# Kernel optimization log

Measured on AMD Instinct MI355X. Metric: run time of the kernel, lower is better.

Reference implementation:

```python
import jax, jax.numpy as jnp
import numpy as np

B, A, C, G = 32, 8732, 201, 50
NEG_TO_POS_RATIO = 3
MIN_NEG_SAMPLES = 0
DET_W, VAL_W = 0.5, 0.5
BOX_W = (10.0, 10.0, 5.0, 5.0)  # torchvision SSD BoxCoder weights


def _rand_boxes(key, shape_prefix):
    k1, k2 = jax.random.split(key)
    cxcy = jax.random.uniform(k1, shape_prefix + (2,)) * 300.0
    wh = jax.random.uniform(k2, shape_prefix + (2,)) * 90.0 + 10.0
    return jnp.concatenate([cxcy - 0.5 * wh, cxcy + 0.5 * wh], axis=-1)


def setup_inputs() -> dict:
    key = jax.random.key(0)
    ks = jax.random.split(key, 8)
    boxes = _rand_boxes(ks[0], (B, G))
    labels = jax.random.randint(ks[1], (B, G), 1, C, dtype=jnp.int32)  # foreground labels > 0
    image_label = jax.random.randint(ks[2], (B,), 0, 2, dtype=jnp.int32)
    bbox_regression = jax.random.normal(ks[3], (B, A, 4), dtype=jnp.float32)
    cls_logits = jax.random.normal(ks[4], (B, A, C), dtype=jnp.float32)
    rejection_logits = jax.random.normal(ks[5], (B, 2), dtype=jnp.float32)
    anchors = _rand_boxes(ks[6], (B, A))
    k7a, k7b = jax.random.split(ks[7])
    fg = jax.random.uniform(k7a, (B, A)) < 0.02
    gt_idx = jax.random.randint(k7b, (B, A), 0, G, dtype=jnp.int32)
    matched_idxs = jnp.where(fg, gt_idx, -1).astype(jnp.int32)
    return {"boxes": boxes, "labels": labels, "image_label": image_label,
            "bbox_regression": bbox_regression, "cls_logits": cls_logits,
            "rejection_logits": rejection_logits, "anchors": anchors,
            "matched_idxs": matched_idxs}


def _encode(gt, anc):
    # torchvision BoxCoder.encode_single with weights (10,10,5,5); boxes are xyxy
    aw = anc[..., 2] - anc[..., 0]
    ah = anc[..., 3] - anc[..., 1]
    acx = anc[..., 0] + 0.5 * aw
    acy = anc[..., 1] + 0.5 * ah
    gw = gt[..., 2] - gt[..., 0]
    gh = gt[..., 3] - gt[..., 1]
    gcx = gt[..., 0] + 0.5 * gw
    gcy = gt[..., 1] + 0.5 * gh
    wx, wy, ww, wh = BOX_W
    return jnp.stack([wx * (gcx - acx) / aw,
                      wy * (gcy - acy) / ah,
                      ww * jnp.log(gw / aw),
                      wh * jnp.log(gh / ah)], axis=-1)


def _forward(boxes, bbox_regression, cls_logits, rejection_logits, anchors,
             labels, image_label, matched_idxs):
    fg = matched_idxs >= 0                                  # [B,A]
    safe = jnp.clip(matched_idxs, 0)                        # in-range gather idx
    num_foreground = fg.sum()

    mg_boxes = jnp.take_along_axis(boxes, safe[..., None], axis=1)  # [B,A,4]
    target_reg = _encode(mg_boxes, anchors)
    d = bbox_regression - target_reg
    ad = jnp.abs(d)
    sl1 = jnp.where(ad < 1.0, 0.5 * d * d, ad - 0.5)        # beta=1.0
    bbox_loss = jnp.sum(sl1 * fg[..., None].astype(sl1.dtype), axis=(1, 2))  # [B]

    # --- classification targets + per-anchor CE ---
    cls_targets = jnp.where(fg, jnp.take_along_axis(labels, safe, axis=1), 0)  # [B,A]
    logp = jax.nn.log_softmax(cls_logits, axis=-1)
    cls_loss = -jnp.take_along_axis(logp, cls_targets[..., None], axis=-1)[..., 0]  # [B,A]

    # --- hard negative mining via double-argsort ranking ---
    fg_mask = cls_targets > 0
    num_neg = NEG_TO_POS_RATIO * fg_mask.sum(axis=1, keepdims=True)
    num_neg = jnp.where(num_neg == 0, MIN_NEG_SAMPLES, num_neg)
    neg_loss = jnp.where(fg_mask, -jnp.inf, cls_loss)
    rank = jnp.argsort(jnp.argsort(-neg_loss, axis=1), axis=1)  # descending rank
    bg_mask = rank < num_neg

    N = jnp.maximum(1, num_foreground).astype(cls_loss.dtype)
    images_without_boxes = (cls_targets.sum(axis=1) == 0).sum()
    N_neg = (MIN_NEG_SAMPLES * images_without_boxes).astype(cls_loss.dtype)

    regression_loss = bbox_loss.sum() / N
    classification_loss = (jnp.sum(jnp.where(fg_mask, cls_loss, 0.0)) +
                           jnp.sum(jnp.where(bg_mask, cls_loss, 0.0))) / (N + N_neg)

    # --- validation head loss ---
    val_logp = jax.nn.log_softmax(rejection_logits, axis=-1)
    validation_loss = -jnp.take_along_axis(val_logp, image_label[:, None], axis=-1).mean()

    loss = DET_W * (regression_loss + classification_loss) + VAL_W * validation_loss
    return jnp.stack([loss, regression_loss, classification_loss, validation_loss])


def reference(boxes, labels, image_label, bbox_regression, cls_logits,
              rejection_logits, anchors, matched_idxs):
    return _forward(boxes, bbox_regression, cls_logits, rejection_logits, anchors,
                    labels, image_label, matched_idxs)
```

## Files before the change

### kernel.cpp

```cpp
#include <hip/hip_runtime.h>
#include <math.h>

#define Bn 32
#define An 8732
#define Cn 201
#define Gn 50

#define RPB 16
#define NTILES ((An + RPB - 1) / RPB)

__device__ __forceinline__ unsigned int f2key(float f) {
    unsigned int u = __float_as_uint(f);
    return (u & 0x80000000u) ? ~u : (u | 0x80000000u);
}
__device__ __forceinline__ float key2f(unsigned int k) {
    return (k & 0x80000000u) ? __uint_as_float(k & 0x7FFFFFFFu) : __uint_as_float(~k);
}
__device__ __forceinline__ float smooth_l1(float d) {
    float ad = fabsf(d);
    return ad < 1.0f ? 0.5f * d * d : ad - 0.5f;
}

__global__ void init_kernel(int* fg_count, float* fg_cls_sum, float* bbox_sum) {
    int i = threadIdx.x;
    if (i < Bn) { fg_count[i] = 0; fg_cls_sum[i] = 0.f; bbox_sum[i] = 0.f; }
}

__global__ __launch_bounds__(256) void cls_kernel(
        const float* __restrict__ cls_logits,
        const int*   __restrict__ matched_idxs,
        const int*   __restrict__ labels,
        const float* __restrict__ boxes,
        const float* __restrict__ anchors,
        const float* __restrict__ bbox_regression,
        float* __restrict__ neg_loss,
        int*   __restrict__ fg_count,
        float* __restrict__ fg_cls_sum,
        float* __restrict__ bbox_sum) {
    __shared__ float tile[RPB * Cn];
    int b     = blockIdx.y;
    int tile0 = blockIdx.x * RPB;
    int rows  = An - tile0; if (rows > RPB) rows = RPB;
    int nvec  = rows * Cn / 4;

    const float4* g  = (const float4*)(cls_logits + ((size_t)b * An + tile0) * Cn);
    float4*       t4 = (float4*)tile;
    for (int i = threadIdx.x; i < nvec; i += 256) t4[i] = g[i];
    __syncthreads();

    int r   = threadIdx.x >> 4;
    int sub = threadIdx.x & 15;
    if (r >= rows) return;
    const float* row = tile + r * Cn;

    float v[13];
    #pragma unroll
    for (int j = 0; j < 12; ++j) v[j] = row[sub + 16 * j];
    bool has12 = (sub < Cn - 192);
    v[12] = has12 ? row[sub + 192] : -INFINITY;

    float mx = v[0];
    #pragma unroll
    for (int j = 1; j < 13; ++j) mx = fmaxf(mx, v[j]);
    #pragma unroll
    for (int off = 8; off; off >>= 1) mx = fmaxf(mx, __shfl_xor(mx, off, 64));

    float s = 0.f;
    #pragma unroll
    for (int j = 0; j < 12; ++j) s += __expf(v[j] - mx);
    if (has12) s += __expf(v[12] - mx);
    #pragma unroll
    for (int off = 8; off; off >>= 1) s += __shfl_xor(s, off, 64);

    if (sub == 0) {
        size_t row_idx = (size_t)b * An + tile0 + r;
        float lse = mx + __logf(s);
        int   mi  = matched_idxs[row_idx];
        bool  fg  = (mi >= 0);
        int   t   = fg ? labels[b * Gn + mi] : 0;
        float cl  = lse - row[t];
        if (fg) {
            neg_loss[row_idx] = -INFINITY;
            atomicAdd(&fg_cls_sum[b], cl);
            atomicAdd(&fg_count[b], 1);
            const float* gt = boxes           + (size_t)(b * Gn + mi) * 4;
            const float* an = anchors         + row_idx * 4;
            const float* rg = bbox_regression + row_idx * 4;
            float aw  = an[2] - an[0], ah  = an[3] - an[1];
            float acx = an[0] + 0.5f * aw, acy = an[1] + 0.5f * ah;
            float gw  = gt[2] - gt[0], gh  = gt[3] - gt[1];
            float gcx = gt[0] + 0.5f * gw, gcy = gt[1] + 0.5f * gh;
            float t0 = 10.f * (gcx - acx) / aw;
            float t1 = 10.f * (gcy - acy) / ah;
            float t2 = 5.f * __logf(gw / aw);
            float t3 = 5.f * __logf(gh / ah);
            float sum = smooth_l1(rg[0] - t0) + smooth_l1(rg[1] - t1)
                      + smooth_l1(rg[2] - t2) + smooth_l1(rg[3] - t3);
            atomicAdd(&bbox_sum[b], sum);
        } else {
            neg_loss[row_idx] = cl;
        }
    }
}

#define MIT 9
__global__ __launch_bounds__(1024) void mining_kernel(
        const float* __restrict__ neg_loss,
        const int*   __restrict__ fg_count,
        float* __restrict__ topk_batch) {
    int b    = blockIdx.x;
    int tid  = threadIdx.x;
    int lane = tid & 63;
    __shared__ int   cnts[32];
    __shared__ float sh_sum;
    __shared__ int   sh_cnt;

    int fc = fg_count[b];
    int k  = 3 * fc;
    int nneg = An - fc;
    if (k > nneg) k = nneg;
    if (k <= 0) {
        if (tid == 0) topk_batch[b] = 0.f;
        return;
    }

    const float* vals = neg_loss + (size_t)b * An;
    unsigned int key[MIT];
    #pragma unroll
    for (int j = 0; j < MIT; ++j) {
        int i = tid + j * 1024;
        key[j] = (i < An) ? f2key(vals[i]) : 0u;
    }

    if (tid < 32) cnts[tid] = 0;
    if (tid == 0) { sh_sum = 0.f; sh_cnt = 0; }
    __syncthreads();

    unsigned int T = 0u;
    for (int bit = 31; bit >= 0; --bit) {
        unsigned int cand = T | (1u << bit);
        int c = 0;
        #pragma unroll
        for (int j = 0; j < MIT; ++j) c += (key[j] >= cand);
        #pragma unroll
        for (int off = 32; off; off >>= 1) c += __shfl_xor(c, off, 64);
        if (lane == 0) atomicAdd(&cnts[bit], c);
        __syncthreads();
        if (cnts[bit] >= k) T = cand;
    }

    float fs = 0.f; int cgt = 0;
    #pragma unroll
    for (int j = 0; j < MIT; ++j)
        if (key[j] > T) { fs += key2f(key[j]); cgt++; }
    #pragma unroll
    for (int off = 32; off; off >>= 1) {
        fs  += __shfl_xor(fs,  off, 64);
        cgt += __shfl_xor(cgt, off, 64);
    }
    if (lane == 0) { atomicAdd(&sh_sum, fs); atomicAdd(&sh_cnt, cgt); }
    __syncthreads();
    if (tid == 0)
        topk_batch[b] = sh_sum + (float)(k - sh_cnt) * key2f(T);
}

__global__ void finalize_kernel(
        const int*   __restrict__ fg_count,
        const float* __restrict__ fg_cls_sum,
        const float* __restrict__ bbox_sum,
        const float* __restrict__ topk_batch,
        const float* __restrict__ rejection_logits,
        const int*   __restrict__ image_label,
        float* __restrict__ out) {
    int lane = threadIdx.x;
    int   fc = (lane < Bn) ? fg_count[lane]   : 0;
    float tk = (lane < Bn) ? topk_batch[lane] : 0.f;
    float cs = (lane < Bn) ? fg_cls_sum[lane] : 0.f;
    float bs = (lane < Bn) ? bbox_sum[lane]   : 0.f;
    float vl = 0.f;
    if (lane < Bn) {
        float r0 = rejection_logits[lane * 2];
        float r1 = rejection_logits[lane * 2 + 1];
        float m  = fmaxf(r0, r1);
        float lse = m + __logf(__expf(r0 - m) + __expf(r1 - m));
        vl = lse - ((image_label[lane] == 0) ? r0 : r1);
    }
    #pragma unroll
    for (int off = 32; off; off >>= 1) {
        fc += __shfl_xor(fc, off, 64);
        tk += __shfl_xor(tk, off, 64);
        cs += __shfl_xor(cs, off, 64);
        bs += __shfl_xor(bs, off, 64);
        vl += __shfl_xor(vl, off, 64);
    }
    if (lane == 0) {
        float N   = (float)((fc > 1) ? fc : 1);
        float reg = bs / N;
        float cls = (cs + tk) / N;
        float val = vl / (float)Bn;
        float loss = 0.5f * (reg + cls) + 0.5f * val;
        out[0] = loss; out[1] = reg; out[2] = cls; out[3] = val;
    }
}

extern "C" void kernel_launch(void* const* d_in, const int* in_sizes, int n_in,
                              void* d_out, int out_size, void* d_ws, size_t ws_size,
                              hipStream_t stream) {
    const float* boxes            = (const float*)d_in[0];
    const int*   labels           = (const int*)  d_in[1];
    const int*   image_label      = (const int*)  d_in[2];
    const float* bbox_regression  = (const float*)d_in[3];
    const float* cls_logits       = (const float*)d_in[4];
    const float* rejection_logits = (const float*)d_in[5];
    const float* anchors          = (const float*)d_in[6];
    const int*   matched_idxs     = (const int*)  d_in[7];
    float* out = (float*)d_out;

    float* neg_loss   = (float*)d_ws;
    int*   fg_count   = (int*)(neg_loss + Bn * An);
    float* fg_cls_sum = (float*)(fg_count + Bn);
    float* bbox_sum   = fg_cls_sum + Bn;
    float* topk_batch = bbox_sum + Bn;

    init_kernel<<<1, 64, 0, stream>>>(fg_count, fg_cls_sum, bbox_sum);

    dim3 grid(NTILES, Bn);
    cls_kernel<<<grid, 256, 0, stream>>>(cls_logits, matched_idxs, labels,
                                         boxes, anchors, bbox_regression,
                                         neg_loss, fg_count, fg_cls_sum, bbox_sum);

    mining_kernel<<<Bn, 1024, 0, stream>>>(neg_loss, fg_count, topk_batch);

    finalize_kernel<<<1, 64, 0, stream>>>(fg_count, fg_cls_sum, bbox_sum, topk_batch,
                                          rejection_logits, image_label, out);
}
```

Measured before the change: 354.1 us.

## Fuse all stages into one persistent cooperative kernel with grid syncs

```diff
diff --git a/kernel.cpp b/kernel.cpp
--- a/kernel.cpp
+++ b/kernel.cpp
@@ -1,5 +1,8 @@
 #include <hip/hip_runtime.h>
+#include <hip/hip_cooperative_groups.h>
 #include <math.h>
+
+namespace cg = cooperative_groups;
 
 #define Bn 32
 #define An 8732
@@ -8,6 +11,9 @@
 
 #define RPB 16
 #define NTILES ((An + RPB - 1) / RPB)
+#define TOTTILES (NTILES * Bn)
+#define GRID 1024
+#define MIT 35
 
 __device__ __forceinline__ unsigned int f2key(float f) {
     unsigned int u = __float_as_uint(f);
@@ -20,217 +26,266 @@
     float ad = fabsf(d);
     return ad < 1.0f ? 0.5f * d * d : ad - 0.5f;
 }
-
-__global__ void init_kernel(int* fg_count, float* fg_cls_sum, float* bbox_sum) {
-    int i = threadIdx.x;
-    if (i < Bn) { fg_count[i] = 0; fg_cls_sum[i] = 0.f; bbox_sum[i] = 0.f; }
-}
-
-__global__ __launch_bounds__(256) void cls_kernel(
+__device__ __forceinline__ void st_u32(unsigned int* p, unsigned int v) {
+    __hip_atomic_store(p, v, __ATOMIC_RELAXED, __HIP_MEMORY_SCOPE_AGENT);
+}
+__device__ __forceinline__ unsigned int ld_u32(const unsigned int* p) {
+    return __hip_atomic_load(p, __ATOMIC_RELAXED, __HIP_MEMORY_SCOPE_AGENT);
+}
+__device__ __forceinline__ void st_i32(int* p, int v) {
+    __hip_atomic_store(p, v, __ATOMIC_RELAXED, __HIP_MEMORY_SCOPE_AGENT);
+}
+__device__ __forceinline__ int ld_i32(const int* p) {
+    return __hip_atomic_load(p, __ATOMIC_RELAXED, __HIP_MEMORY_SCOPE_AGENT);
+}
+__device__ __forceinline__ void st_f32(float* p, float v) {
+    __hip_atomic_store(p, v, __ATOMIC_RELAXED, __HIP_MEMORY_SCOPE_AGENT);
+}
+__device__ __forceinline__ float ld_f32(const float* p) {
+    return __hip_atomic_load(p, __ATOMIC_RELAXED, __HIP_MEMORY_SCOPE_AGENT);
+}
+
+__global__ __launch_bounds__(256, 4) void fused_kernel(
         const float* __restrict__ cls_logits,
         const int*   __restrict__ matched_idxs,
         const int*   __restrict__ labels,
         const float* __restrict__ boxes,
         const float* __restrict__ anchors,
         const float* __restrict__ bbox_regression,
-        float* __restrict__ neg_loss,
-        int*   __restrict__ fg_count,
-        float* __restrict__ fg_cls_sum,
-        float* __restrict__ bbox_sum) {
+        const float* __restrict__ rejection_logits,
+        const int*   __restrict__ image_label,
+        unsigned int* neg_key,
+        int*   slot_cnt,
+        float* slot_cls,
+        float* slot_bbox,
+        int*   batch_fc,
+        float* batch_cls,
+        float* batch_bbox,
+        float* topk,
+        float* out) {
     __shared__ float tile[RPB * Cn];
-    int b     = blockIdx.y;
-    int tile0 = blockIdx.x * RPB;
-    int rows  = An - tile0; if (rows > RPB) rows = RPB;
-    int nvec  = rows * Cn / 4;
-
-    const float4* g  = (const float4*)(cls_logits + ((size_t)b * An + tile0) * Cn);
-    float4*       t4 = (float4*)tile;
-    for (int i = threadIdx.x; i < nvec; i += 256) t4[i] = g[i];
-    __syncthreads();
-
-    int r   = threadIdx.x >> 4;
-    int sub = threadIdx.x & 15;
-    if (r >= rows) return;
-    const float* row = tile + r * Cn;
-
-    float v[13];
-    #pragma unroll
-    for (int j = 0; j < 12; ++j) v[j] = row[sub + 16 * j];
-    bool has12 = (sub < Cn - 192);
-    v[12] = has12 ? row[sub + 192] : -INFINITY;
-
-    float mx = v[0];
-    #pragma unroll
-    for (int j = 1; j < 13; ++j) mx = fmaxf(mx, v[j]);
-    #pragma unroll
-    for (int off = 8; off; off >>= 1) mx = fmaxf(mx, __shfl_xor(mx, off, 64));
-
-    float s = 0.f;
-    #pragma unroll
-    for (int j = 0; j < 12; ++j) s += __expf(v[j] - mx);
-    if (has12) s += __expf(v[12] - mx);
-    #pragma unroll
-    for (int off = 8; off; off >>= 1) s += __shfl_xor(s, off, 64);
-
-    if (sub == 0) {
-        size_t row_idx = (size_t)b * An + tile0 + r;
-        float lse = mx + __logf(s);
-        int   mi  = matched_idxs[row_idx];
-        bool  fg  = (mi >= 0);
-        int   t   = fg ? labels[b * Gn + mi] : 0;
-        float cl  = lse - row[t];
-        if (fg) {
-            neg_loss[row_idx] = -INFINITY;
-            atomicAdd(&fg_cls_sum[b], cl);
-            atomicAdd(&fg_count[b], 1);
-            const float* gt = boxes           + (size_t)(b * Gn + mi) * 4;
-            const float* an = anchors         + row_idx * 4;
-            const float* rg = bbox_regression + row_idx * 4;
-            float aw  = an[2] - an[0], ah  = an[3] - an[1];
-            float acx = an[0] + 0.5f * aw, acy = an[1] + 0.5f * ah;
-            float gw  = gt[2] - gt[0], gh  = gt[3] - gt[1];
-            float gcx = gt[0] + 0.5f * gw, gcy = gt[1] + 0.5f * gh;
-            float t0 = 10.f * (gcx - acx) / aw;
-            float t1 = 10.f * (gcy - acy) / ah;
-            float t2 = 5.f * __logf(gw / aw);
-            float t3 = 5.f * __logf(gh / ah);
-            float sum = smooth_l1(rg[0] - t0) + smooth_l1(rg[1] - t1)
-                      + smooth_l1(rg[2] - t2) + smooth_l1(rg[3] - t3);
-            atomicAdd(&bbox_sum[b], sum);
-        } else {
-            neg_loss[row_idx] = cl;
-        }
-    }
-}
-
-#define MIT 9
-__global__ __launch_bounds__(1024) void mining_kernel(
-        const float* __restrict__ neg_loss,
-        const int*   __restrict__ fg_count,
-        float* __restrict__ topk_batch) {
-    int b    = blockIdx.x;
+    __shared__ int   p_cnt[Bn];
+    __shared__ float p_cls[Bn];
+    __shared__ float p_bbox[Bn];
+    __shared__ int   cnts[32];
+    __shared__ int   red_i;
+    __shared__ float red_f1, red_f2;
+
+    cg::grid_group gridg = cg::this_grid();
+    int bid  = blockIdx.x;
     int tid  = threadIdx.x;
     int lane = tid & 63;
-    __shared__ int   cnts[32];
-    __shared__ float sh_sum;
-    __shared__ int   sh_cnt;
-
-    int fc = fg_count[b];
-    int k  = 3 * fc;
-    int nneg = An - fc;
-    if (k > nneg) k = nneg;
-    if (k <= 0) {
-        if (tid == 0) topk_batch[b] = 0.f;
-        return;
-    }
-
-    const float* vals = neg_loss + (size_t)b * An;
-    unsigned int key[MIT];
-    #pragma unroll
-    for (int j = 0; j < MIT; ++j) {
-        int i = tid + j * 1024;
-        key[j] = (i < An) ? f2key(vals[i]) : 0u;
-    }
-
-    if (tid < 32) cnts[tid] = 0;
-    if (tid == 0) { sh_sum = 0.f; sh_cnt = 0; }
+
+    if (tid < Bn) { p_cnt[tid] = 0; p_cls[tid] = 0.f; p_bbox[tid] = 0.f; }
+
+    int r   = tid >> 4;
+    int sub = tid & 15;
+
+    for (int t = bid; t < TOTTILES; t += GRID) {
+        int b     = t / NTILES;
+        int tile0 = (t % NTILES) * RPB;
+        int rows  = An - tile0; if (rows > RPB) rows = RPB;
+        int nvec  = rows * Cn / 4;
+        __syncthreads();
+        const float4* g = (const float4*)(cls_logits + ((size_t)b * An + tile0) * Cn);
+        for (int i = tid; i < nvec; i += 256) ((float4*)tile)[i] = g[i];
+        __syncthreads();
+        if (r < rows) {
+            const float* row = tile + r * Cn;
+            float v[13];
+            #pragma unroll
+            for (int j = 0; j < 12; ++j) v[j] = row[sub + 16 * j];
+            bool has12 = (sub < Cn - 192);
+            v[12] = has12 ? row[sub + 192] : -INFINITY;
+
+            float mx = v[0];
+            #pragma unroll
+            for (int j = 1; j < 13; ++j) mx = fmaxf(mx, v[j]);
+            #pragma unroll
+            for (int off = 8; off; off >>= 1) mx = fmaxf(mx, __shfl_xor(mx, off, 64));
+
+            float s = 0.f;
+            #pragma unroll
+            for (int j = 0; j < 12; ++j) s += __expf(v[j] - mx);
+            if (has12) s += __expf(v[12] - mx);
+            #pragma unroll
+            for (int off = 8; off; off >>= 1) s += __shfl_xor(s, off, 64);
+
+            if (sub == 0) {
+                size_t row_idx = (size_t)b * An + tile0 + r;
+                float lse = mx + __logf(s);
+                int   mi  = matched_idxs[row_idx];
+                if (mi >= 0) {
+                    int   tl = labels[b * Gn + mi];
+                    float cl = lse - row[tl];
+                    st_u32(&neg_key[row_idx], 0u);
+                    atomicAdd(&p_cnt[b], 1);
+                    atomicAdd(&p_cls[b], cl);
+                    const float* gt = boxes           + (size_t)(b * Gn + mi) * 4;
+                    const float* an = anchors         + row_idx * 4;
+                    const float* rg = bbox_regression + row_idx * 4;
+                    float aw  = an[2] - an[0], ah  = an[3] - an[1];
+                    float acx = an[0] + 0.5f * aw, acy = an[1] + 0.5f * ah;
+                    float gw  = gt[2] - gt[0], gh  = gt[3] - gt[1];
+                    float gcx = gt[0] + 0.5f * gw, gcy = gt[1] + 0.5f * gh;
+                    float t0 = 10.f * (gcx - acx) / aw;
+                    float t1 = 10.f * (gcy - acy) / ah;
+                    float t2 = 5.f * __logf(gw / aw);
+                    float t3 = 5.f * __logf(gh / ah);
+                    float sm = smooth_l1(rg[0] - t0) + smooth_l1(rg[1] - t1)
+                             + smooth_l1(rg[2] - t2) + smooth_l1(rg[3] - t3);
+                    atomicAdd(&p_bbox[b], sm);
+                } else {
+                    float cl = lse - row[0];
+                    st_u32(&neg_key[row_idx], f2key(cl));
+                }
+            }
+        }
+    }
     __syncthreads();
-
-    unsigned int T = 0u;
-    for (int bit = 31; bit >= 0; --bit) {
-        unsigned int cand = T | (1u << bit);
-        int c = 0;
+    if (tid < Bn) {
+        st_i32(&slot_cnt [tid * GRID + bid], p_cnt[tid]);
+        st_f32(&slot_cls [tid * GRID + bid], p_cls[tid]);
+        st_f32(&slot_bbox[tid * GRID + bid], p_bbox[tid]);
+    }
+    __threadfence();
+    gridg.sync();
+
+    if (bid < Bn) {
+        int b = bid;
+        int fc = 0; float cs = 0.f, bs = 0.f;
+        for (int i = tid; i < GRID; i += 256) {
+            fc += ld_i32(&slot_cnt [b * GRID + i]);
+            cs += ld_f32(&slot_cls [b * GRID + i]);
+            bs += ld_f32(&slot_bbox[b * GRID + i]);
+        }
         #pragma unroll
-        for (int j = 0; j < MIT; ++j) c += (key[j] >= cand);
+        for (int off = 32; off; off >>= 1) {
+            fc += __shfl_xor(fc, off, 64);
+            cs += __shfl_xor(cs, off, 64);
+            bs += __shfl_xor(bs, off, 64);
+        }
+        if (tid == 0) { red_i = 0; red_f1 = 0.f; red_f2 = 0.f; }
+        __syncthreads();
+        if (lane == 0) {
+            atomicAdd(&red_i, fc);
+            atomicAdd(&red_f1, cs);
+            atomicAdd(&red_f2, bs);
+        }
+        __syncthreads();
+        fc = red_i;
+        if (tid == 0) {
+            st_i32(&batch_fc[b], fc);
+            st_f32(&batch_cls[b], red_f1);
+            st_f32(&batch_bbox[b], red_f2);
+        }
+        int k = 3 * fc;
+        int nneg = An - fc;
+        if (k > nneg) k = nneg;
+        if (k <= 0) {
+            if (tid == 0) st_f32(&topk[b], 0.f);
+        } else {
+            unsigned int key[MIT];
+            #pragma unroll
+            for (int j = 0; j < MIT; ++j) {
+                int i = tid + j * 256;
+                key[j] = (i < An) ? ld_u32(&neg_key[(size_t)b * An + i]) : 0u;
+            }
+            if (tid < 32) cnts[tid] = 0;
+            __syncthreads();
+            unsigned int T = 0u;
+            for (int bit = 31; bit >= 0; --bit) {
+                unsigned int cand = T | (1u << bit);
+                int c = 0;
+                #pragma unroll
+                for (int j = 0; j < MIT; ++j) c += (key[j] >= cand);
+                #pragma unroll
+                for (int off = 32; off; off >>= 1) c += __shfl_xor(c, off, 64);
+                if (lane == 0) atomicAdd(&cnts[bit], c);
+                __syncthreads();
+                if (cnts[bit] >= k) T = cand;
+            }
+            float fs = 0.f; int cgt = 0;
+            #pragma unroll
+            for (int j = 0; j < MIT; ++j)
+                if (key[j] > T) { fs += key2f(key[j]); cgt++; }
+            #pragma unroll
+            for (int off = 32; off; off >>= 1) {
+                fs  += __shfl_xor(fs,  off, 64);
+                cgt += __shfl_xor(cgt, off, 64);
+            }
+            if (tid == 0) { red_f1 = 0.f; red_i = 0; }
+            __syncthreads();
+            if (lane == 0) { atomicAdd(&red_f1, fs); atomicAdd(&red_i, cgt); }
+            __syncthreads();
+            if (tid == 0)
+                st_f32(&topk[b], red_f1 + (float)(k - red_i) * key2f(T));
+        }
+    }
+    __threadfence();
+    gridg.sync();
+
+    if (bid == 0 && tid < 64) {
+        int   fc = (lane < Bn) ? ld_i32(&batch_fc[lane])   : 0;
+        float tk = (lane < Bn) ? ld_f32(&topk[lane])       : 0.f;
+        float cs = (lane < Bn) ? ld_f32(&batch_cls[lane])  : 0.f;
+        float bs = (lane < Bn) ? ld_f32(&batch_bbox[lane]) : 0.f;
+        float vl = 0.f;
+        if (lane < Bn) {
+            float r0 = rejection_logits[lane * 2];
+            float r1 = rejection_logits[lane * 2 + 1];
+            float m  = fmaxf(r0, r1);
+            float lse = m + __logf(__expf(r0 - m) + __expf(r1 - m));
+            vl = lse - ((image_label[lane] == 0) ? r0 : r1);
+        }
         #pragma unroll
-        for (int off = 32; off; off >>= 1) c += __shfl_xor(c, off, 64);
-        if (lane == 0) atomicAdd(&cnts[bit], c);
-        __syncthreads();
-        if (cnts[bit] >= k) T = cand;
-    }
-
-    float fs = 0.f; int cgt = 0;
-    #pragma unroll
-    for (int j = 0; j < MIT; ++j)
-        if (key[j] > T) { fs += key2f(key[j]); cgt++; }
-    #pragma unroll
-    for (int off = 32; off; off >>= 1) {
-        fs  += __shfl_xor(fs,  off, 64);
-        cgt += __shfl_xor(cgt, off, 64);
-    }
-    if (lane == 0) { atomicAdd(&sh_sum, fs); atomicAdd(&sh_cnt, cgt); }
-    __syncthreads();
-    if (tid == 0)
-        topk_batch[b] = sh_sum + (float)(k - sh_cnt) * key2f(T);
-}
-
-__global__ void finalize_kernel(
-        const int*   __restrict__ fg_count,
-        const float* __restrict__ fg_cls_sum,
-        const float* __restrict__ bbox_sum,
-        const float* __restrict__ topk_batch,
-        const float* __restrict__ rejection_logits,
-        const int*   __restrict__ image_label,
-        float* __restrict__ out) {
-    int lane = threadIdx.x;
-    int   fc = (lane < Bn) ? fg_count[lane]   : 0;
-    float tk = (lane < Bn) ? topk_batch[lane] : 0.f;
-    float cs = (lane < Bn) ? fg_cls_sum[lane] : 0.f;
-    float bs = (lane < Bn) ? bbox_sum[lane]   : 0.f;
-    float vl = 0.f;
-    if (lane < Bn) {
-        float r0 = rejection_logits[lane * 2];
-        float r1 = rejection_logits[lane * 2 + 1];
-        float m  = fmaxf(r0, r1);
-        float lse = m + __logf(__expf(r0 - m) + __expf(r1 - m));
-        vl = lse - ((image_label[lane] == 0) ? r0 : r1);
-    }
-    #pragma unroll
-    for (int off = 32; off; off >>= 1) {
-        fc += __shfl_xor(fc, off, 64);
-        tk += __shfl_xor(tk, off, 64);
-        cs += __shfl_xor(cs, off, 64);
-        bs += __shfl_xor(bs, off, 64);
-        vl += __shfl_xor(vl, off, 64);
-    }
-    if (lane == 0) {
-        float N   = (float)((fc > 1) ? fc : 1);
-        float reg = bs / N;
-        float cls = (cs + tk) / N;
-        float val = vl / (float)Bn;
-        float loss = 0.5f * (reg + cls) + 0.5f * val;
-        out[0] = loss; out[1] = reg; out[2] = cls; out[3] = val;
+        for (int off = 32; off; off >>= 1) {
+            fc += __shfl_xor(fc, off, 64);
+            tk += __shfl_xor(tk, off, 64);
+            cs += __shfl_xor(cs, off, 64);
+            bs += __shfl_xor(bs, off, 64);
+            vl += __shfl_xor(vl, off, 64);
+        }
+        if (lane == 0) {
+            float N   = (float)((fc > 1) ? fc : 1);
+            float reg = bs / N;
+            float cls = (cs + tk) / N;
+            float val = vl / (float)Bn;
+            out[0] = 0.5f * (reg + cls) + 0.5f * val;
+            out[1] = reg; out[2] = cls; out[3] = val;
+        }
     }
 }
 
 extern "C" void kernel_launch(void* const* d_in, const int* in_sizes, int n_in,
                               void* d_out, int out_size, void* d_ws, size_t ws_size,
                               hipStream_t stream) {
+    const float* cls_logits       = (const float*)d_in[4];
+    const int*   matched_idxs     = (const int*)  d_in[7];
+    const int*   labels           = (const int*)  d_in[1];
     const float* boxes            = (const float*)d_in[0];
-    const int*   labels           = (const int*)  d_in[1];
+    const float* anchors          = (const float*)d_in[6];
+    const float* bbox_regression  = (const float*)d_in[3];
+    const float* rejection_logits = (const float*)d_in[5];
     const int*   image_label      = (const int*)  d_in[2];
-    const float* bbox_regression  = (const float*)d_in[3];
-    const float* cls_logits       = (const float*)d_in[4];
-    const float* rejection_logits = (const float*)d_in[5];
-    const float* anchors          = (const float*)d_in[6];
-    const int*   matched_idxs     = (const int*)  d_in[7];
     float* out = (float*)d_out;
 
-    float* neg_loss   = (float*)d_ws;
-    int*   fg_count   = (int*)(neg_loss + Bn * An);
-    float* fg_cls_sum = (float*)(fg_count + Bn);
-    float* bbox_sum   = fg_cls_sum + Bn;
-    float* topk_batch = bbox_sum + Bn;
-
-    init_kernel<<<1, 64, 0, stream>>>(fg_count, fg_cls_sum, bbox_sum);
-
-    dim3 grid(NTILES, Bn);
-    cls_kernel<<<grid, 256, 0, stream>>>(cls_logits, matched_idxs, labels,
-                                         boxes, anchors, bbox_regression,
-                                         neg_loss, fg_count, fg_cls_sum, bbox_sum);
-
-    mining_kernel<<<Bn, 1024, 0, stream>>>(neg_loss, fg_count, topk_batch);
-
-    finalize_kernel<<<1, 64, 0, stream>>>(fg_count, fg_cls_sum, bbox_sum, topk_batch,
-                                          rejection_logits, image_label, out);
-}
+    unsigned int* neg_key = (unsigned int*)d_ws;
+    int*   slot_cnt   = (int*)(neg_key + (size_t)Bn * An);
+    float* slot_cls   = (float*)(slot_cnt + Bn * GRID);
+    float* slot_bbox  = slot_cls + Bn * GRID;
+    int*   batch_fc   = (int*)(slot_bbox + Bn * GRID);
+    float* batch_cls  = (float*)(batch_fc + Bn);
+    float* batch_bbox = batch_cls + Bn;
+    float* topk       = batch_bbox + Bn;
+
+    void* args[] = {
+        (void*)&cls_logits, (void*)&matched_idxs, (void*)&labels, (void*)&boxes,
+        (void*)&anchors, (void*)&bbox_regression, (void*)&rejection_logits,
+        (void*)&image_label, (void*)&neg_key, (void*)&slot_cnt, (void*)&slot_cls,
+        (void*)&slot_bbox, (void*)&batch_fc, (void*)&batch_cls, (void*)&batch_bbox,
+        (void*)&topk, (void*)&out
+    };
+    hipLaunchCooperativeKernel((void*)fused_kernel, dim3(GRID), dim3(256),
+                               args, 0, stream);
+}
```

Measured after the change: 752.0 us. +112.3%, slower.
